# Performance work log

Hardware: AMD Instinct MI355X
Metric: run time of the kernel (lower is better)

The kernel has to match this reference:

```python
import jax, jax.numpy as jnp
import numpy as np

N_HEADS = 16


def apply_rotary_emb(x, cos, sin):
    # x: [B, H, S, hd]; cos/sin: [S, hd//2] (broadcast over B, H)
    xr = x.reshape(x.shape[:-1] + (-1, 2))
    r, i = xr[..., 0], xr[..., 1]
    a = r * cos - i * sin
    b = i * cos + r * sin
    return jnp.stack([a, b], axis=-1).reshape(x.shape).astype(x.dtype)


def setup_inputs() -> dict:
    key = jax.random.key(0)
    ks = jax.random.split(key, 7)
    B, S, D = 2, 2048, 1024
    hd = D // N_HEADS
    x = jax.random.normal(ks[0], (B, S, D), dtype=jnp.float32)
    freqs_cos = jax.random.uniform(ks[1], (S, hd // 2), dtype=jnp.float32)
    freqs_sin = jax.random.uniform(ks[2], (S, hd // 2), dtype=jnp.float32)
    sc = 1.0 / np.sqrt(D)
    Wq = jax.random.normal(ks[3], (D, D), dtype=jnp.float32) * sc
    Wk = jax.random.normal(ks[4], (D, D), dtype=jnp.float32) * sc
    Wv = jax.random.normal(ks[5], (D, D), dtype=jnp.float32) * sc
    Wo = jax.random.normal(ks[6], (D, D), dtype=jnp.float32) * sc
    return {"x": x, "freqs_cos": freqs_cos, "freqs_sin": freqs_sin,
            "Wq": Wq, "Wk": Wk, "Wv": Wv, "Wo": Wo}


def reference(x, freqs_cos, freqs_sin, Wq, Wk, Wv, Wo):
    B, S, D = x.shape
    H = N_HEADS
    hd = D // H
    # QKV projections (nn.Linear: x @ W.T)
    q = (x @ Wq.T).reshape(B, S, H, hd).transpose(0, 2, 1, 3)
    k = (x @ Wk.T).reshape(B, S, H, hd).transpose(0, 2, 1, 3)
    v = (x @ Wv.T).reshape(B, S, H, hd).transpose(0, 2, 1, 3)
    q = apply_rotary_emb(q, freqs_cos, freqs_sin)
    k = apply_rotary_emb(k, freqs_cos, freqs_sin)
    # causal SDPA (scale = 1/sqrt(head_dim), as in F.scaled_dot_product_attention)
    scores = jnp.einsum("bhqd,bhkd->bhqk", q, k) * (1.0 / np.sqrt(hd))
    causal = jnp.tril(jnp.ones((S, S), dtype=bool))
    scores = jnp.where(causal, scores, -jnp.inf)
    probs = jax.nn.softmax(scores, axis=-1)
    attn_out = jnp.einsum("bhqk,bhkd->bhqd", probs, v)
    attn_cat = attn_out.transpose(0, 2, 1, 3).reshape(B, S, D)
    return attn_cat @ Wo.T
```

## Files before the change

kernel.cpp:

```cpp
#include <hip/hip_runtime.h>
#include <hip/hip_bf16.h>
#include <cstdint>

typedef __attribute__((ext_vector_type(8))) short short8;
typedef __attribute__((ext_vector_type(4))) float f32x4;

#define B_  2
#define S_  2048
#define D_  1024
#define H_  16
#define HD  64

static __device__ __forceinline__ float bf2f(unsigned int u16) {
    union { unsigned int i; float f; } v; v.i = u16 << 16; return v.f;
}
static __device__ __forceinline__ unsigned short f2bf(float f) {
    union { float f; unsigned int i; } v; v.f = f;
    unsigned int r = v.i + 0x7FFFu + ((v.i >> 16) & 1u);
    return (unsigned short)(r >> 16);
}
static __device__ __forceinline__ unsigned pack_bf16(float hi, float lo) {
    union { float f; unsigned u; } h, l;
    h.f = hi; l.f = lo;
    return __builtin_amdgcn_perm(h.u + 0x8000u, l.u + 0x8000u, 0x07060302);
}
static __device__ __forceinline__ void load_lds_16B(const unsigned short* g, unsigned short* l) {
    __builtin_amdgcn_global_load_lds(
        (const __attribute__((address_space(1))) unsigned int*)g,
        (__attribute__((address_space(3))) unsigned int*)l, 16, 0, 0);
}

__global__ void cvt_all(const float* __restrict__ x,
                        const float* __restrict__ w0, const float* __restrict__ w1,
                        const float* __restrict__ w2, const float* __restrict__ w3,
                        unsigned short* __restrict__ xbf,
                        unsigned short* __restrict__ wdst) {
    int bid = blockIdx.x;
    if (bid < 4096) {
        int i = bid * 256 + threadIdx.x;
        float4 f = ((const float4*)x)[i];
        uint2 o;
        o.x = (unsigned int)f2bf(f.x) | ((unsigned int)f2bf(f.y) << 16);
        o.y = (unsigned int)f2bf(f.z) | ((unsigned int)f2bf(f.w) << 16);
        ((uint2*)xbf)[i] = o;
    } else {
        int wb = bid - 4096;
        int wsel = wb >> 10;
        const float* s = wsel == 0 ? w0 : wsel == 1 ? w1 : wsel == 2 ? w2 : w3;
        int i = (wb & 1023) * 256 + threadIdx.x;
        float4 f = ((const float4*)s)[i];
        uint2 o;
        o.x = (unsigned int)f2bf(f.x) | ((unsigned int)f2bf(f.y) << 16);
        o.y = (unsigned int)f2bf(f.z) | ((unsigned int)f2bf(f.w) << 16);
        ((uint2*)wdst)[(size_t)wsel * 262144 + i] = o;
    }
}

__global__ __launch_bounds__(256) void qkv_gemm(
    const unsigned short* __restrict__ xbf,
    const unsigned short* __restrict__ wq,
    const unsigned short* __restrict__ wk,
    const unsigned short* __restrict__ wv,
    const float* __restrict__ fcos,
    const float* __restrict__ fsin,
    unsigned short* __restrict__ qb,
    unsigned short* __restrict__ kb,
    unsigned short* __restrict__ vb)
{
    __shared__ unsigned short As[128 * 32];
    __shared__ unsigned short Bs[128 * 32];

    const int tid  = threadIdx.x;
    const int w    = tid >> 6, lane = tid & 63;
    const int l15  = lane & 15, quad = lane >> 4;
    const int wrow = (w >> 1) * 64, wcol = (w & 1) * 64;

    const int m0 = blockIdx.x * 128;
    const int nc = blockIdx.y * 128;
    const int sel = nc >> 10;
    const int n0 = nc & 1023;
    const unsigned short* __restrict__ W = sel == 0 ? wq : (sel == 1 ? wk : wv);

    const int lr = lane >> 2, lc = (lane & 3) * 8;
    const unsigned short* ga = xbf + (size_t)(m0 + w * 16 + lr) * 1024 + lc;
    const unsigned short* gb = W   + (size_t)(n0 + w * 16 + lr) * 1024 + lc;
    unsigned short* la0 = As + (w * 16) * 32;
    unsigned short* la1 = As + (64 + w * 16) * 32;
    unsigned short* lb0 = Bs + (w * 16) * 32;
    unsigned short* lb1 = Bs + (64 + w * 16) * 32;

    f32x4 acc[4][4] = {};

    for (int k0 = 0; k0 < 1024; k0 += 32) {
        __syncthreads();
        load_lds_16B(ga + k0,             la0);
        load_lds_16B(ga + 64 * 1024 + k0, la1);
        load_lds_16B(gb + k0,             lb0);
        load_lds_16B(gb + 64 * 1024 + k0, lb1);
        __syncthreads();

        short8 a[4], b[4];
#pragma unroll
        for (int i = 0; i < 4; i++)
            a[i] = *(const short8*)&As[(wrow + i * 16 + l15) * 32 + quad * 8];
#pragma unroll
        for (int j = 0; j < 4; j++)
            b[j] = *(const short8*)&Bs[(wcol + j * 16 + l15) * 32 + quad * 8];
#pragma unroll
        for (int i = 0; i < 4; i++)
#pragma unroll
            for (int j = 0; j < 4; j++)
                acc[i][j] = __builtin_amdgcn_mfma_f32_16x16x32_bf16(a[i], b[j], acc[i][j], 0, 0, 0);
    }

    if (sel == 2) {
#pragma unroll
        for (int i = 0; i < 4; i++)
#pragma unroll
            for (int r = 0; r < 4; r++) {
                int m = m0 + wrow + i * 16 + quad * 4 + r;
                int bb = m >> 11, s = m & 2047;
#pragma unroll
                for (int j = 0; j < 4; j++) {
                    int n = n0 + wcol + j * 16 + l15;
                    int h = n >> 6, d = n & 63;
                    vb[(((size_t)(bb * H_ + h)) * HD + d) * S_ + s] = f2bf(acc[i][j][r]);
                }
            }
    } else {
        unsigned short* __restrict__ Out = sel == 0 ? qb : kb;
        const float qsc = (sel == 0) ? 0.125f * 1.44269504f : 1.0f;
        const int odd = l15 & 1;
#pragma unroll
        for (int i = 0; i < 4; i++)
#pragma unroll
            for (int r = 0; r < 4; r++) {
                int m = m0 + wrow + i * 16 + quad * 4 + r;
                int bb = m >> 11, s = m & 2047;
#pragma unroll
                for (int j = 0; j < 4; j++) {
                    int n = n0 + wcol + j * 16 + l15;
                    int h = n >> 6, d = n & 63;
                    int t = d >> 1;
                    float c  = fcos[s * 32 + t];
                    float si = fsin[s * 32 + t];
                    float own = acc[i][j][r];
                    float oth = __shfl_xor(own, 1, 64);
                    float outv = odd ? (own * c + oth * si) : (own * c - oth * si);
                    Out[(((size_t)(bb * H_ + h) * S_) + s) * HD + d] = f2bf(outv * qsc);
                }
            }
    }
}

__global__ __launch_bounds__(256) void out_gemm(
    const unsigned short* __restrict__ A,
    const unsigned short* __restrict__ Bt,
    float* __restrict__ C)
{
    __shared__ unsigned short As[128 * 32];
    __shared__ unsigned short Bs[128 * 32];

    const int tid  = threadIdx.x;
    const int w    = tid >> 6, lane = tid & 63;
    const int l15  = lane & 15, quad = lane >> 4;
    const int wrow = (w >> 1) * 64, wcol = (w & 1) * 64;

    const int m0 = blockIdx.x * 128;
    const int n0 = blockIdx.y * 128;

    const int lr = lane >> 2, lc = (lane & 3) * 8;
    const unsigned short* ga = A  + (size_t)(m0 + w * 16 + lr) * 1024 + lc;
    const unsigned short* gb = Bt + (size_t)(n0 + w * 16 + lr) * 1024 + lc;
    unsigned short* la0 = As + (w * 16) * 32;
    unsigned short* la1 = As + (64 + w * 16) * 32;
    unsigned short* lb0 = Bs + (w * 16) * 32;
    unsigned short* lb1 = Bs + (64 + w * 16) * 32;

    f32x4 acc[4][4] = {};

    for (int k0 = 0; k0 < 1024; k0 += 32) {
        __syncthreads();
        load_lds_16B(ga + k0,             la0);
        load_lds_16B(ga + 64 * 1024 + k0, la1);
        load_lds_16B(gb + k0,             lb0);
        load_lds_16B(gb + 64 * 1024 + k0, lb1);
        __syncthreads();

        short8 a[4], b[4];
#pragma unroll
        for (int i = 0; i < 4; i++)
            a[i] = *(const short8*)&As[(wrow + i * 16 + l15) * 32 + quad * 8];
#pragma unroll
        for (int j = 0; j < 4; j++)
            b[j] = *(const short8*)&Bs[(wcol + j * 16 + l15) * 32 + quad * 8];
#pragma unroll
        for (int i = 0; i < 4; i++)
#pragma unroll
            for (int j = 0; j < 4; j++)
                acc[i][j] = __builtin_amdgcn_mfma_f32_16x16x32_bf16(a[i], b[j], acc[i][j], 0, 0, 0);
    }

#pragma unroll
    for (int i = 0; i < 4; i++)
#pragma unroll
        for (int r = 0; r < 4; r++) {
            int m = m0 + wrow + i * 16 + quad * 4 + r;
#pragma unroll
            for (int j = 0; j < 4; j++)
                C[(size_t)m * 1024 + n0 + wcol + j * 16 + l15] = acc[i][j][r];
        }
}

__global__ __launch_bounds__(256) void flash_attn_mfma(
    const unsigned short* __restrict__ qb,
    const unsigned short* __restrict__ kb,
    const unsigned short* __restrict__ vT,
    unsigned short* __restrict__ attnc)
{
    __shared__ __attribute__((aligned(1024))) unsigned short Ks[2][2][64][32];
    __shared__ __attribute__((aligned(1024))) unsigned short Vt[64][64];
    __shared__ unsigned short Pls[4][16][72];

    const int bh   = blockIdx.x;
    const int qtb  = blockIdx.y;
    const int jj = qtb & 7, mm = qtb >> 3;
    const int qt = (mm == 0) ? jj : (mm == 1) ? 31 - jj : (mm == 2) ? 8 + jj : 23 - jj;

    const int b    = bh >> 4, h = bh & 15;
    const int tid  = threadIdx.x;
    const int w    = tid >> 6;
    const int lane = tid & 63;
    const int l15  = lane & 15;
    const int quad = lane >> 4;

    const size_t bhS = (size_t)bh * S_;
    const unsigned short* __restrict__ vTb = vT + (size_t)bh * HD * S_;

    short8 qfrag[2];
    {
        const unsigned short* qp = qb + (bhS + qt * 64 + w * 16 + l15) * HD + quad * 8;
        qfrag[0] = *(const short8*)(qp);
        qfrag[1] = *(const short8*)(qp + 32);
    }

    const int ksrow  = lane >> 2;
    const int ksslot = (lane & 3) ^ ((lane >> 3) & 3);
    const int vsrow  = lane >> 3;
    const int vsslot = (lane & 7) ^ vsrow;

    const int ckq = (quad ^ ((l15 >> 1) & 3)) << 4;
    const int s7  = l15 & 7;

    short8 ones;
#pragma unroll
    for (int i = 0; i < 8; i++) ones[i] = (short)0x3F80;

    f32x4 O[4] = {};
    f32x4 Osum = {};
    float mrow = -INFINITY;

    auto STAGE_K = [&](int jt, int bufi) {
        const int j0 = jt * 64;
        const unsigned short* kg = kb + (bhS + j0 + w * 16 + ksrow) * HD + ksslot * 8;
        load_lds_16B(kg,      &Ks[bufi][0][w * 16][0]);
        load_lds_16B(kg + 32, &Ks[bufi][1][w * 16][0]);
    };
    auto STAGE_V = [&](int jt) {
        const int j0 = jt * 64;
        const unsigned short* vg = vTb + (size_t)(w * 16 + vsrow) * S_ + j0 + vsslot * 8;
        load_lds_16B(vg,          &Vt[w * 16][0]);
        load_lds_16B(vg + 8 * S_, &Vt[w * 16 + 8][0]);
    };

    STAGE_K(0, 0);

    for (int jt = 0; jt <= qt; jt++) {
        const int cur = jt & 1;
        if (jt < qt) {
            STAGE_K(jt + 1, cur ^ 1);
            STAGE_V(jt);
            asm volatile("s_waitcnt vmcnt(4)" ::: "memory");
        } else {
            STAGE_V(jt);
            asm volatile("s_waitcnt vmcnt(2)" ::: "memory");
        }
        __builtin_amdgcn_s_barrier();

        const bool diag  = (jt == qt);
        const int  nsub  = diag ? (w + 1) : 4;
        const int  kgmax = (nsub + 1) >> 1;

        f32x4 Sacc[4];
        float tmax = -INFINITY;
        for (int sub = 0; sub < nsub; sub++) {
            f32x4 s = {};
#pragma unroll
            for (int kh = 0; kh < 2; kh++) {
                int bo = ((sub * 16 + l15) << 6) + ckq;
                short8 kf = *(const short8*)((const char*)&Ks[cur][kh][0][0] + bo);
                s = __builtin_amdgcn_mfma_f32_16x16x32_bf16(kf, qfrag[kh], s, 0, 0, 0);
            }
#pragma unroll
            for (int r = 0; r < 4; r++) {
                float v = s[r];
                if (diag && (sub * 16 + quad * 4 + r > w * 16 + l15)) v = -INFINITY;
                s[r] = v;
                tmax = fmaxf(tmax, v);
            }
            Sacc[sub] = s;
        }
        tmax = fmaxf(tmax, __shfl_xor(tmax, 16, 64));
        tmax = fmaxf(tmax, __shfl_xor(tmax, 32, 64));

        if (__any(tmax > mrow + 8.0f)) {
            float mnew = fmaxf(mrow, tmax);
            float ccr  = __builtin_amdgcn_exp2f(mrow - mnew);
#pragma unroll
            for (int r = 0; r < 4; r++) {
                float ccq = __shfl(ccr, quad * 4 + r, 64);
#pragma unroll
                for (int dt = 0; dt < 4; dt++) O[dt][r] *= ccq;
                Osum[r] *= ccq;
            }
            mrow = mnew;
        }

        for (int sub = 0; sub < nsub; sub++) {
            f32x4 s = Sacc[sub];
            float p0 = __builtin_amdgcn_exp2f(s[0] - mrow);
            float p1 = __builtin_amdgcn_exp2f(s[1] - mrow);
            float p2 = __builtin_amdgcn_exp2f(s[2] - mrow);
            float p3 = __builtin_amdgcn_exp2f(s[3] - mrow);
            uint2 pk;
            pk.x = pack_bf16(p1, p0);
            pk.y = pack_bf16(p3, p2);
            *(uint2*)&Pls[w][l15][sub * 16 + quad * 4] = pk;
        }
        if (diag) {
            for (int sub = nsub; sub < 2 * kgmax; sub++) {
                uint2 z; z.x = 0u; z.y = 0u;
                *(uint2*)&Pls[w][l15][sub * 16 + quad * 4] = z;
            }
        }

        if (jt < qt) {
            asm volatile("s_waitcnt vmcnt(2)" ::: "memory");
        } else {
            asm volatile("s_waitcnt vmcnt(0)" ::: "memory");
        }
        __builtin_amdgcn_s_barrier();

        for (int kg = 0; kg < kgmax; kg++) {
            short8 pf = *(const short8*)&Pls[w][l15][kg * 32 + quad * 8];
#pragma unroll
            for (int dt = 0; dt < 4; dt++) {
                int row = dt * 16 + l15;
                int slot = (((kg << 2) | quad) ^ s7) << 4;
                short8 vf = *(const short8*)((const char*)&Vt[0][0] + (row << 7) + slot);
                O[dt] = __builtin_amdgcn_mfma_f32_16x16x32_bf16(pf, vf, O[dt], 0, 0, 0);
            }
            Osum = __builtin_amdgcn_mfma_f32_16x16x32_bf16(pf, ones, Osum, 0, 0, 0);
        }

        asm volatile("" ::: "memory");
        __builtin_amdgcn_s_barrier();
    }

#pragma unroll
    for (int r = 0; r < 4; r++) {
        float invq = 1.0f / Osum[r];
        int qabs = qt * 64 + w * 16 + quad * 4 + r;
        unsigned short* op = attnc + (((size_t)b * S_ + qabs) * H_ + h) * HD + l15;
#pragma unroll
        for (int dt = 0; dt < 4; dt++)
            op[dt * 16] = f2bf(O[dt][r] * invq);
    }
}

extern "C" void kernel_launch(void* const* d_in, const int* in_sizes, int n_in,
                              void* d_out, int out_size, void* d_ws, size_t ws_size,
                              hipStream_t stream) {
    const float* x    = (const float*)d_in[0];
    const float* fcos = (const float*)d_in[1];
    const float* fsin = (const float*)d_in[2];
    const float* Wq   = (const float*)d_in[3];
    const float* Wk   = (const float*)d_in[4];
    const float* Wv   = (const float*)d_in[5];
    const float* Wo   = (const float*)d_in[6];
    float* out = (float*)d_out;

    unsigned short* ws = (unsigned short*)d_ws;
    unsigned short* xbf = ws;
    unsigned short* wqb = xbf + 4096 * 1024;
    unsigned short* wkb = wqb + 1024 * 1024;
    unsigned short* wvb = wkb + 1024 * 1024;
    unsigned short* wob = wvb + 1024 * 1024;
    unsigned short* qb  = wob + 1024 * 1024;
    unsigned short* kb  = qb + 4096 * 1024;
    unsigned short* vb  = kb + 4096 * 1024;
    unsigned short* attnc = vb + 4096 * 1024;

    cvt_all<<<8192, 256, 0, stream>>>(x, Wq, Wk, Wv, Wo, xbf, wqb);

    qkv_gemm<<<dim3(32, 24), 256, 0, stream>>>(xbf, wqb, wkb, wvb, fcos, fsin, qb, kb, vb);

    flash_attn_mfma<<<dim3(32, 32), 256, 0, stream>>>(qb, kb, vb, attnc);

    out_gemm<<<dim3(32, 8), 256, 0, stream>>>(attnc, wob, out);
}
```

Before: 219.6 us.

## Stage V transpose through LDS and halve out_gemm N tile

```diff
diff --git a/kernel.cpp b/kernel.cpp
--- a/kernel.cpp
+++ b/kernel.cpp
@@ -69,6 +69,7 @@
 {
     __shared__ unsigned short As[128 * 32];
     __shared__ unsigned short Bs[128 * 32];
+    __shared__ unsigned short Tt[64][136];
 
     const int tid  = threadIdx.x;
     const int w    = tid >> 6, lane = tid & 63;
@@ -114,19 +115,34 @@
     }
 
     if (sel == 2) {
-#pragma unroll
-        for (int i = 0; i < 4; i++)
-#pragma unroll
-            for (int r = 0; r < 4; r++) {
-                int m = m0 + wrow + i * 16 + quad * 4 + r;
-                int bb = m >> 11, s = m & 2047;
-#pragma unroll
-                for (int j = 0; j < 4; j++) {
-                    int n = n0 + wcol + j * 16 + l15;
-                    int h = n >> 6, d = n & 63;
-                    vb[(((size_t)(bb * H_ + h)) * HD + d) * S_ + s] = f2bf(acc[i][j][r]);
-                }
-            }
+        const int bb  = blockIdx.x >> 4;
+        const int m0s = (blockIdx.x & 15) * 128;
+        const int h0  = n0 >> 6;
+        const int nh  = w & 1;
+#pragma unroll
+        for (int half = 0; half < 2; half++) {
+            __syncthreads();
+            if (nh == half) {
+#pragma unroll
+                for (int i = 0; i < 4; i++)
+#pragma unroll
+                    for (int j = 0; j < 4; j++) {
+                        uint2 pk;
+                        pk.x = pack_bf16(acc[i][j][1], acc[i][j][0]);
+                        pk.y = pack_bf16(acc[i][j][3], acc[i][j][2]);
+                        *(uint2*)&Tt[j * 16 + l15][wrow + i * 16 + quad * 4] = pk;
+                    }
+            }
+            __syncthreads();
+            const int row = tid >> 2, cq = tid & 3;
+            unsigned short* vrow = vb +
+                (((size_t)(bb * H_ + h0 + half)) * HD + row) * S_ + m0s + cq * 32;
+#pragma unroll
+            for (int k = 0; k < 4; k++) {
+                short8 v = *(const short8*)&Tt[row][cq * 32 + k * 8];
+                *(short8*)(vrow + k * 8) = v;
+            }
+        }
     } else {
         unsigned short* __restrict__ Out = sel == 0 ? qb : kb;
         const float qsc = (sel == 0) ? 0.125f * 1.44269504f : 1.0f;
@@ -159,15 +175,15 @@
     float* __restrict__ C)
 {
     __shared__ unsigned short As[128 * 32];
-    __shared__ unsigned short Bs[128 * 32];
+    __shared__ unsigned short Bs[64 * 32];
 
     const int tid  = threadIdx.x;
     const int w    = tid >> 6, lane = tid & 63;
     const int l15  = lane & 15, quad = lane >> 4;
-    const int wrow = (w >> 1) * 64, wcol = (w & 1) * 64;
+    const int wrow = (w >> 1) * 64, wcol = (w & 1) * 32;
 
     const int m0 = blockIdx.x * 128;
-    const int n0 = blockIdx.y * 128;
+    const int n0 = blockIdx.y * 64;
 
     const int lr = lane >> 2, lc = (lane & 3) * 8;
     const unsigned short* ga = A  + (size_t)(m0 + w * 16 + lr) * 1024 + lc;
@@ -175,29 +191,27 @@
     unsigned short* la0 = As + (w * 16) * 32;
     unsigned short* la1 = As + (64 + w * 16) * 32;
     unsigned short* lb0 = Bs + (w * 16) * 32;
-    unsigned short* lb1 = Bs + (64 + w * 16) * 32;
-
-    f32x4 acc[4][4] = {};
+
+    f32x4 acc[4][2] = {};
 
     for (int k0 = 0; k0 < 1024; k0 += 32) {
         __syncthreads();
         load_lds_16B(ga + k0,             la0);
         load_lds_16B(ga + 64 * 1024 + k0, la1);
         load_lds_16B(gb + k0,             lb0);
-        load_lds_16B(gb + 64 * 1024 + k0, lb1);
         __syncthreads();
 
-        short8 a[4], b[4];
+        short8 a[4], b[2];
 #pragma unroll
         for (int i = 0; i < 4; i++)
             a[i] = *(const short8*)&As[(wrow + i * 16 + l15) * 32 + quad * 8];
 #pragma unroll
-        for (int j = 0; j < 4; j++)
+        for (int j = 0; j < 2; j++)
             b[j] = *(const short8*)&Bs[(wcol + j * 16 + l15) * 32 + quad * 8];
 #pragma unroll
         for (int i = 0; i < 4; i++)
 #pragma unroll
-            for (int j = 0; j < 4; j++)
+            for (int j = 0; j < 2; j++)
                 acc[i][j] = __builtin_amdgcn_mfma_f32_16x16x32_bf16(a[i], b[j], acc[i][j], 0, 0, 0);
     }
 
@@ -207,7 +221,7 @@
         for (int r = 0; r < 4; r++) {
             int m = m0 + wrow + i * 16 + quad * 4 + r;
 #pragma unroll
-            for (int j = 0; j < 4; j++)
+            for (int j = 0; j < 2; j++)
                 C[(size_t)m * 1024 + n0 + wcol + j * 16 + l15] = acc[i][j][r];
         }
 }
@@ -407,5 +421,5 @@
 
     flash_attn_mfma<<<dim3(32, 32), 256, 0, stream>>>(qb, kb, vb, attnc);
 
-    out_gemm<<<dim3(32, 8), 256, 0, stream>>>(attnc, wob, out);
-}
+    out_gemm<<<dim3(32, 16), 256, 0, stream>>>(attnc, wob, out);
+}
```

New measurement: 216.2 us. No clear change (-1.5%).
